# Kernel tuning notes

Measured on AMD Instinct MI355X. Metric: run time of the kernel, lower is better.

Reference implementation:

```python
import jax, jax.numpy as jnp
import numpy as np

B, S, D, H = 2, 2048, 1024, 16
ND = D // H  # head dim = 64


def setup_inputs() -> dict:
    key = jax.random.key(0)
    ks = jax.random.split(key, 11)
    scale = 1.0 / np.sqrt(D)
    inp = {
        "q": jax.random.normal(ks[0], (B, S, D), dtype=jnp.float32),
        "k": jax.random.normal(ks[1], (B, S, D), dtype=jnp.float32),
        "v": jax.random.normal(ks[2], (B, S, D), dtype=jnp.float32),
        # causal mask, broadcast over batch and heads
        "mask": jnp.tril(jnp.ones((S, S), dtype=jnp.int32))[None, None, :, :],
        "Wq": jax.random.normal(ks[3], (D, D), dtype=jnp.float32) * scale,
        "bq": jnp.zeros((D,), dtype=jnp.float32),
        "Wk": jax.random.normal(ks[4], (D, D), dtype=jnp.float32) * scale,
        "bk": jnp.zeros((D,), dtype=jnp.float32),
        "Wv": jax.random.normal(ks[5], (D, D), dtype=jnp.float32) * scale,
        "bv": jnp.zeros((D,), dtype=jnp.float32),
        "Wo": jax.random.normal(ks[6], (D, D), dtype=jnp.float32) * scale,
        "bo": jnp.zeros((D,), dtype=jnp.float32),
    }
    return inp


def reference(q, k, v, mask, Wq, bq, Wk, bk, Wv, bv, Wo, bo):
    batch, seq_len, _ = q.shape
    # torch nn.Linear: x @ W.T + b
    qh = (q @ Wq.T + bq).reshape(batch, seq_len, H, ND).transpose(0, 2, 1, 3)
    kh = (k @ Wk.T + bk).reshape(batch, seq_len, H, ND).transpose(0, 2, 1, 3)
    vh = (v @ Wv.T + bv).reshape(batch, seq_len, H, ND).transpose(0, 2, 1, 3)
    # [B,H,S,S] scores
    score = jnp.einsum("bhqd,bhkd->bhqk", qh, kh) / jnp.sqrt(jnp.float32(ND))
    score = jnp.where(mask == 0, jnp.float32(-1e9), score)
    score = jax.nn.softmax(score, axis=-1)
    out = jnp.einsum("bhqk,bhkd->bhqd", score, vh)
    out = out.transpose(0, 2, 1, 3).reshape(batch, seq_len, D)
    return out @ Wo.T + bo
```

## Files before the change

kernel.cpp:

```cpp
#include <hip/hip_runtime.h>
#include <hip/hip_bf16.h>
#include <stdint.h>

#define S_LEN 2048
#define DMODEL 1024
#define NHEAD 16
#define HDIM 64
#define BATCH 2

typedef __bf16 bf16_t;
typedef __attribute__((ext_vector_type(8))) __bf16 bf16x8;
typedef __attribute__((ext_vector_type(4))) __bf16 bf16x4;
typedef __attribute__((ext_vector_type(4))) float f32x4;

#define LOG2E 1.44269504088896340736f

__device__ __forceinline__ void gload_lds16(const void* g, void* l) {
  __builtin_amdgcn_global_load_lds(
      (const __attribute__((address_space(1))) uint32_t*)g,
      (__attribute__((address_space(3))) uint32_t*)l, 16, 0, 0);
}

__global__ __launch_bounds__(256) void convert_all(
    const float* __restrict__ q, const float* __restrict__ k, const float* __restrict__ v,
    const float* __restrict__ wq, const float* __restrict__ wk, const float* __restrict__ wv,
    const float* __restrict__ wo,
    bf16_t* __restrict__ qb, bf16_t* __restrict__ kb, bf16_t* __restrict__ vb,
    bf16_t* __restrict__ wqb, bf16_t* __restrict__ wkb, bf16_t* __restrict__ wvb,
    bf16_t* __restrict__ wob)
{
  const size_t M1 = 1048576;
  size_t e = ((size_t)blockIdx.x * 256 + threadIdx.x) * 4;
  const float* src; bf16_t* dst; size_t off;
  if      (e <  4*M1) { src = q;  dst = qb;  off = e;         }
  else if (e <  8*M1) { src = k;  dst = kb;  off = e - 4*M1;  }
  else if (e < 12*M1) { src = v;  dst = vb;  off = e - 8*M1;  }
  else if (e < 13*M1) { src = wq; dst = wqb; off = e - 12*M1; }
  else if (e < 14*M1) { src = wk; dst = wkb; off = e - 13*M1; }
  else if (e < 15*M1) { src = wv; dst = wvb; off = e - 14*M1; }
  else                { src = wo; dst = wob; off = e - 15*M1; }
  float4 f = *reinterpret_cast<const float4*>(src + off);
  bf16x4 o;
  o[0] = (bf16_t)f.x; o[1] = (bf16_t)f.y; o[2] = (bf16_t)f.z; o[3] = (bf16_t)f.w;
  *reinterpret_cast<bf16x4*>(dst + off) = o;
}

__device__ __forceinline__ void gemm_body(
    const bf16_t* __restrict__ A, const bf16_t* __restrict__ W,
    const float* __restrict__ bias, bf16_t* __restrict__ outb,
    float* __restrict__ outf, int M, int N, int K, float scale, int kpack)
{
  __shared__ bf16_t As[128 * 32];
  __shared__ bf16_t Bs[128 * 32];
  int tid = threadIdx.x;
  int w = tid >> 6, lane = tid & 63;
  int lr = lane & 15, lg = lane >> 4;
  int wr = w >> 1, wc = w & 1;
  int m0 = blockIdx.x * 128, n0 = blockIdx.y * 128;

  f32x4 acc[4][4];
#pragma unroll
  for (int a = 0; a < 4; ++a)
#pragma unroll
    for (int bq = 0; bq < 4; ++bq) acc[a][bq] = (f32x4){0.f, 0.f, 0.f, 0.f};

  int col_st = (lane & 3) * 8;

  for (int kt = 0; kt < K; kt += 32) {
#pragma unroll
    for (int it = 0; it < 2; ++it) {
      int chunkbase = (w * 2 + it) * 512;
      int row = (w * 2 + it) * 16 + (lane >> 2);
      gload_lds16(A + (size_t)(m0 + row) * K + kt + col_st, &As[chunkbase]);
      gload_lds16(W + (size_t)(n0 + row) * K + kt + col_st, &Bs[chunkbase]);
    }
    __syncthreads();
    bf16x8 af[4], bfv[4];
#pragma unroll
    for (int mf = 0; mf < 4; ++mf)
      af[mf] = *reinterpret_cast<const bf16x8*>(&As[(wr * 64 + mf * 16 + lr) * 32 + lg * 8]);
#pragma unroll
    for (int nf = 0; nf < 4; ++nf)
      bfv[nf] = *reinterpret_cast<const bf16x8*>(&Bs[(wc * 64 + nf * 16 + lr) * 32 + lg * 8]);
#pragma unroll
    for (int mf = 0; mf < 4; ++mf)
#pragma unroll
      for (int nf = 0; nf < 4; ++nf)
        acc[mf][nf] = __builtin_amdgcn_mfma_f32_16x16x32_bf16(af[mf], bfv[nf], acc[mf][nf], 0, 0, 0);
    __syncthreads();
  }

#pragma unroll
  for (int mf = 0; mf < 4; ++mf) {
#pragma unroll
    for (int nf = 0; nf < 4; ++nf) {
      int col = n0 + wc * 64 + nf * 16 + lr;
      float bcol = bias[col];
#pragma unroll
      for (int i = 0; i < 4; ++i) {
        int row = m0 + wr * 64 + mf * 16 + lg * 4 + i;
        float vv = (acc[mf][nf][i] + bcol) * scale;
        if (outf) {
          outf[(size_t)row * N + col] = vv;
        } else if (!kpack) {
          outb[(size_t)row * N + col] = (bf16_t)vv;
        } else {
          int hh = col >> 6, dh = col & 63;
          int half = dh >> 5, klg = (dh >> 3) & 3, j = dh & 7;
          int bb = row >> 11, s = row & 2047;
          size_t off = ((((size_t)(bb * 16 + hh) * 32 + (s >> 6)) * 4 + ((s >> 4) & 3)) * 2 + half) * 512
                     + (klg * 16 + (s & 15)) * 8 + j;
          outb[off] = (bf16_t)vv;
        }
      }
    }
  }
}

__global__ __launch_bounds__(256) void gemm_proj(
    const bf16_t* __restrict__ qb, const bf16_t* __restrict__ kb, const bf16_t* __restrict__ vb,
    const bf16_t* __restrict__ wqb, const bf16_t* __restrict__ wkb, const bf16_t* __restrict__ wvb,
    const float* __restrict__ bq, const float* __restrict__ bk, const float* __restrict__ bv,
    bf16_t* __restrict__ Qp, bf16_t* __restrict__ Kpk, bf16_t* __restrict__ Vp)
{
  int z = blockIdx.z;
  const bf16_t* A = (z == 0) ? qb : (z == 1) ? kb : vb;
  const bf16_t* W = (z == 0) ? wqb : (z == 1) ? wkb : wvb;
  const float* bias = (z == 0) ? bq : (z == 1) ? bk : bv;
  bf16_t* o = (z == 0) ? Qp : (z == 1) ? Kpk : Vp;
  float scale = (z == 0) ? 0.125f * LOG2E : 1.0f;
  gemm_body(A, W, bias, o, nullptr, BATCH * S_LEN, DMODEL, DMODEL, scale, z == 1);
}

__global__ __launch_bounds__(256) void gemm_out(
    const bf16_t* __restrict__ O, const bf16_t* __restrict__ wob,
    const float* __restrict__ bo, float* __restrict__ out)
{
  gemm_body(O, wob, bo, nullptr, out, BATCH * S_LEN, DMODEL, DMODEL, 1.0f, 0);
}

__global__ __launch_bounds__(256) void transpose_v(
    const bf16_t* __restrict__ Vp, bf16_t* __restrict__ Vpk)
{
  int bh = blockIdx.y, b = bh >> 4, h = bh & 15;
  int s0 = blockIdx.x * 64;
  __shared__ bf16_t lt[64 * 72];
  int tid = threadIdx.x;
  int c0 = (tid & 7) * 8;
#pragma unroll
  for (int it = 0; it < 2; ++it) {
    int rr = (tid >> 3) + it * 32;
    *reinterpret_cast<bf16x8*>(&lt[rr * 72 + c0]) =
        *reinterpret_cast<const bf16x8*>(Vp + ((size_t)b * S_LEN + s0 + rr) * DMODEL + h * HDIM + c0);
  }
  __syncthreads();
#pragma unroll
  for (int it = 0; it < 2; ++it) {
    int d = (tid >> 3) + it * 32;
    int sc = (tid & 7) * 8;
    bf16x8 o;
#pragma unroll
    for (int j = 0; j < 8; ++j) o[j] = lt[(sc + j) * 72 + d];
    int dfo = d >> 4, vlr = d & 15;
    int half = sc >> 5, vlg = (sc >> 3) & 3;
    size_t off = (((size_t)bh * 32 + blockIdx.x) * 8 + dfo * 2 + half) * 512
               + (vlg * 16 + vlr) * 8;
    *reinterpret_cast<bf16x8*>(Vpk + off) = o;
  }
}

#define PSTRIDE 66

__global__ __launch_bounds__(512, 4) void attn_fwd(
    const bf16_t* __restrict__ Qp, const bf16_t* __restrict__ Kpk,
    const bf16_t* __restrict__ Vpk, bf16_t* __restrict__ O)
{
  int flat = blockIdx.x;
  int low = flat & 7, kk = flat >> 3;
  int pj = kk & 15;
  int bh = ((kk >> 4) << 3) + low;
  int b = bh >> 4, h = bh & 15;
  int tid = threadIdx.x, wv = tid >> 6, lane = tid & 63;
  int lr = lane & 15, lg = lane >> 4;
  int grp = wv >> 2, wl = wv & 3;
  int qt = grp ? (31 - pj) : pj;

  __shared__ bf16_t Ps[8][16 * PSTRIDE];

  int q_row = qt * 64 + wl * 16 + lr;
  const bf16_t* Qbase = Qp + ((size_t)b * S_LEN + q_row) * DMODEL + h * HDIM + lg * 8;
  bf16x8 qf0 = *reinterpret_cast<const bf16x8*>(Qbase);
  bf16x8 qf1 = *reinterpret_cast<const bf16x8*>(Qbase + 32);

  f32x4 oacc[4];
#pragma unroll
  for (int df = 0; df < 4; ++df) oacc[df] = (f32x4){0.f, 0.f, 0.f, 0.f};
  float m = -1e30f, l = 0.f;

  const bf16_t* Kb = Kpk + (size_t)bh * (32 * 4096) + lane * 8;
  const bf16_t* Vb = Vpk + (size_t)bh * (32 * 4096) + lane * 8;
  bf16_t* ps = &Ps[wv][lr * PSTRIDE];

  for (int t = 0; t <= qt; ++t) {
    const bf16_t* Kt = Kb + t * 4096;
    const bf16_t* Vt_ = Vb + t * 4096;

    f32x4 sacc[4];
#pragma unroll
    for (int kvf = 0; kvf < 4; ++kvf) {
      bf16x8 kf0 = *reinterpret_cast<const bf16x8*>(Kt + (kvf * 2 + 0) * 512);
      bf16x8 kf1 = *reinterpret_cast<const bf16x8*>(Kt + (kvf * 2 + 1) * 512);
      f32x4 s = (f32x4){0.f, 0.f, 0.f, 0.f};
      s = __builtin_amdgcn_mfma_f32_16x16x32_bf16(kf0, qf0, s, 0, 0, 0);
      s = __builtin_amdgcn_mfma_f32_16x16x32_bf16(kf1, qf1, s, 0, 0, 0);
      sacc[kvf] = s;
    }

    bf16x8 vf[4][2];
#pragma unroll
    for (int dfo = 0; dfo < 4; ++dfo) {
      vf[dfo][0] = *reinterpret_cast<const bf16x8*>(Vt_ + (dfo * 2 + 0) * 512);
      vf[dfo][1] = *reinterpret_cast<const bf16x8*>(Vt_ + (dfo * 2 + 1) * 512);
    }

    if (t == qt) {
      int kv0 = t * 64;
#pragma unroll
      for (int kvf = 0; kvf < 4; ++kvf) {
        int kv_g = kv0 + kvf * 16 + lg * 4;
#pragma unroll
        for (int i = 0; i < 4; ++i)
          if (kv_g + i > q_row) sacc[kvf][i] = -1e30f;
      }
    }

    float lmax = fmaxf(fmaxf(sacc[0][0], sacc[0][1]), fmaxf(sacc[0][2], sacc[0][3]));
#pragma unroll
    for (int kvf = 1; kvf < 4; ++kvf)
      lmax = fmaxf(lmax, fmaxf(fmaxf(sacc[kvf][0], sacc[kvf][1]),
                               fmaxf(sacc[kvf][2], sacc[kvf][3])));
    if (__any(lmax > m + 8.f)) {
      float mx = lmax;
      mx = fmaxf(mx, __shfl_xor(mx, 16));
      mx = fmaxf(mx, __shfl_xor(mx, 32));
      float mn = fmaxf(m, mx);
      float rr = __builtin_amdgcn_exp2f(m - mn);
      m = mn; l *= rr;
#pragma unroll
      for (int dfo = 0; dfo < 4; ++dfo) oacc[dfo] *= rr;
    }

    float psum = 0.f;
#pragma unroll
    for (int kvf = 0; kvf < 4; ++kvf) {
      bf16x4 pw;
#pragma unroll
      for (int i = 0; i < 4; ++i) {
        float p = __builtin_amdgcn_exp2f(sacc[kvf][i] - m);
        psum += p;
        pw[i] = (bf16_t)p;
      }
      *reinterpret_cast<bf16x4*>(ps + kvf * 16 + lg * 4) = pw;
    }
    l += psum;

    asm volatile("s_waitcnt lgkmcnt(0)" ::: "memory");
    __builtin_amdgcn_sched_barrier(0);

    bf16x8 pa0 = *reinterpret_cast<const bf16x8*>(ps + lg * 8);
    bf16x8 pa1 = *reinterpret_cast<const bf16x8*>(ps + 32 + lg * 8);
#pragma unroll
    for (int dfo = 0; dfo < 4; ++dfo) {
      oacc[dfo] = __builtin_amdgcn_mfma_f32_16x16x32_bf16(vf[dfo][0], pa0, oacc[dfo], 0, 0, 0);
      oacc[dfo] = __builtin_amdgcn_mfma_f32_16x16x32_bf16(vf[dfo][1], pa1, oacc[dfo], 0, 0, 0);
    }
  }

  l += __shfl_xor(l, 16);
  l += __shfl_xor(l, 32);
  float inv = 1.0f / l;
  bf16_t* ob = O + ((size_t)b * S_LEN + q_row) * DMODEL + h * HDIM + lg * 4;
#pragma unroll
  for (int dfo = 0; dfo < 4; ++dfo) {
    bf16x4 ov;
#pragma unroll
    for (int i = 0; i < 4; ++i) ov[i] = (bf16_t)(oacc[dfo][i] * inv);
    *reinterpret_cast<bf16x4*>(ob + dfo * 16) = ov;
  }
}

extern "C" void kernel_launch(void* const* d_in, const int* in_sizes, int n_in,
                              void* d_out, int out_size, void* d_ws, size_t ws_size,
                              hipStream_t stream) {
  const float* q  = (const float*)d_in[0];
  const float* k  = (const float*)d_in[1];
  const float* v  = (const float*)d_in[2];
  const float* Wq = (const float*)d_in[4];
  const float* bq = (const float*)d_in[5];
  const float* Wk = (const float*)d_in[6];
  const float* bk = (const float*)d_in[7];
  const float* Wv = (const float*)d_in[8];
  const float* bv = (const float*)d_in[9];
  const float* Wo = (const float*)d_in[10];
  const float* bo = (const float*)d_in[11];
  float* out = (float*)d_out;

  const size_t MB = 1u << 20;
  char* base = (char*)d_ws;
  bf16_t* qb  = (bf16_t*)(base + 0 * MB);
  bf16_t* kb  = (bf16_t*)(base + 8 * MB);
  bf16_t* vb  = (bf16_t*)(base + 16 * MB);
  bf16_t* wqb = (bf16_t*)(base + 24 * MB);
  bf16_t* wkb = (bf16_t*)(base + 26 * MB);
  bf16_t* wvb = (bf16_t*)(base + 28 * MB);
  bf16_t* wob = (bf16_t*)(base + 30 * MB);
  bf16_t* Qp  = (bf16_t*)(base + 32 * MB);
  bf16_t* Kpk = (bf16_t*)(base + 40 * MB);
  bf16_t* Vp  = (bf16_t*)(base + 48 * MB);
  bf16_t* Vpk = (bf16_t*)(base + 56 * MB);
  bf16_t* Ob  = (bf16_t*)(base + 64 * MB);

  convert_all<<<16384, 256, 0, stream>>>(q, k, v, Wq, Wk, Wv, Wo,
                                         qb, kb, vb, wqb, wkb, wvb, wob);
  gemm_proj<<<dim3(32, 8, 3), 256, 0, stream>>>(qb, kb, vb, wqb, wkb, wvb,
                                                bq, bk, bv, Qp, Kpk, Vp);
  transpose_v<<<dim3(32, 32), 256, 0, stream>>>(Vp, Vpk);
  attn_fwd<<<512, 512, 0, stream>>>(Qp, Kpk, Vpk, Ob);
  gemm_out<<<dim3(32, 8), 256, 0, stream>>>(Ob, wob, bo, out);
}
```

Baseline: 134.8 us.

## Fuse V transpose into projection epilogue and prefetch K tiles in attention

The V projection GEMM now writes directly in the packed, transposed layout the attention kernel consumes, which removes the separate transpose_v kernel launch and its extra read/write of V. The attention loop also prefetches the next K tile into registers during softmax, so the load latency is hidden, and it raises wave priority around the MFMA blocks. The fused epilogue does scattered 2-byte stores with poor coalescing, and the K prefetch adds register pressure under a 4-waves launch bound.

```diff
diff --git a/kernel.cpp b/kernel.cpp
--- a/kernel.cpp
+++ b/kernel.cpp
@@ -48,7 +48,7 @@
 __device__ __forceinline__ void gemm_body(
     const bf16_t* __restrict__ A, const bf16_t* __restrict__ W,
     const float* __restrict__ bias, bf16_t* __restrict__ outb,
-    float* __restrict__ outf, int M, int N, int K, float scale, int kpack)
+    float* __restrict__ outf, int M, int N, int K, float scale, int packmode)
 {
   __shared__ bf16_t As[128 * 32];
   __shared__ bf16_t Bs[128 * 32];
@@ -102,15 +102,24 @@
         float vv = (acc[mf][nf][i] + bcol) * scale;
         if (outf) {
           outf[(size_t)row * N + col] = vv;
-        } else if (!kpack) {
+        } else if (packmode == 0) {
           outb[(size_t)row * N + col] = (bf16_t)vv;
-        } else {
+        } else if (packmode == 1) {
           int hh = col >> 6, dh = col & 63;
           int half = dh >> 5, klg = (dh >> 3) & 3, j = dh & 7;
           int bb = row >> 11, s = row & 2047;
           size_t off = ((((size_t)(bb * 16 + hh) * 32 + (s >> 6)) * 4 + ((s >> 4) & 3)) * 2 + half) * 512
                      + (klg * 16 + (s & 15)) * 8 + j;
           outb[off] = (bf16_t)vv;
+        } else {
+          int hh = col >> 6, d = col & 63;
+          int dfo = d >> 4, vlr = d & 15;
+          int bb = row >> 11, s = row & 2047;
+          int t64 = s >> 6, sin_ = s & 63;
+          int half = sin_ >> 5, vlg = (sin_ >> 3) & 3, j = s & 7;
+          size_t off = (((size_t)(bb * 16 + hh) * 32 + t64) * 8 + dfo * 2 + half) * 512
+                     + (vlg * 16 + vlr) * 8 + j;
+          outb[off] = (bf16_t)vv;
         }
       }
     }
@@ -121,15 +130,15 @@
     const bf16_t* __restrict__ qb, const bf16_t* __restrict__ kb, const bf16_t* __restrict__ vb,
     const bf16_t* __restrict__ wqb, const bf16_t* __restrict__ wkb, const bf16_t* __restrict__ wvb,
     const float* __restrict__ bq, const float* __restrict__ bk, const float* __restrict__ bv,
-    bf16_t* __restrict__ Qp, bf16_t* __restrict__ Kpk, bf16_t* __restrict__ Vp)
+    bf16_t* __restrict__ Qp, bf16_t* __restrict__ Kpk, bf16_t* __restrict__ Vpk)
 {
   int z = blockIdx.z;
   const bf16_t* A = (z == 0) ? qb : (z == 1) ? kb : vb;
   const bf16_t* W = (z == 0) ? wqb : (z == 1) ? wkb : wvb;
   const float* bias = (z == 0) ? bq : (z == 1) ? bk : bv;
-  bf16_t* o = (z == 0) ? Qp : (z == 1) ? Kpk : Vp;
+  bf16_t* o = (z == 0) ? Qp : (z == 1) ? Kpk : Vpk;
   float scale = (z == 0) ? 0.125f * LOG2E : 1.0f;
-  gemm_body(A, W, bias, o, nullptr, BATCH * S_LEN, DMODEL, DMODEL, scale, z == 1);
+  gemm_body(A, W, bias, o, nullptr, BATCH * S_LEN, DMODEL, DMODEL, scale, z);
 }
 
 __global__ __launch_bounds__(256) void gemm_out(
@@ -137,36 +146,6 @@
     const float* __restrict__ bo, float* __restrict__ out)
 {
   gemm_body(O, wob, bo, nullptr, out, BATCH * S_LEN, DMODEL, DMODEL, 1.0f, 0);
-}
-
-__global__ __launch_bounds__(256) void transpose_v(
-    const bf16_t* __restrict__ Vp, bf16_t* __restrict__ Vpk)
-{
-  int bh = blockIdx.y, b = bh >> 4, h = bh & 15;
-  int s0 = blockIdx.x * 64;
-  __shared__ bf16_t lt[64 * 72];
-  int tid = threadIdx.x;
-  int c0 = (tid & 7) * 8;
-#pragma unroll
-  for (int it = 0; it < 2; ++it) {
-    int rr = (tid >> 3) + it * 32;
-    *reinterpret_cast<bf16x8*>(&lt[rr * 72 + c0]) =
-        *reinterpret_cast<const bf16x8*>(Vp + ((size_t)b * S_LEN + s0 + rr) * DMODEL + h * HDIM + c0);
-  }
-  __syncthreads();
-#pragma unroll
-  for (int it = 0; it < 2; ++it) {
-    int d = (tid >> 3) + it * 32;
-    int sc = (tid & 7) * 8;
-    bf16x8 o;
-#pragma unroll
-    for (int j = 0; j < 8; ++j) o[j] = lt[(sc + j) * 72 + d];
-    int dfo = d >> 4, vlr = d & 15;
-    int half = sc >> 5, vlg = (sc >> 3) & 3;
-    size_t off = (((size_t)bh * 32 + blockIdx.x) * 8 + dfo * 2 + half) * 512
-               + (vlg * 16 + vlr) * 8;
-    *reinterpret_cast<bf16x8*>(Vpk + off) = o;
-  }
 }
 
 #define PSTRIDE 66
@@ -201,27 +180,31 @@
   const bf16_t* Vb = Vpk + (size_t)bh * (32 * 4096) + lane * 8;
   bf16_t* ps = &Ps[wv][lr * PSTRIDE];
 
+  bf16x8 kc[8];
+  {
+    const bf16_t* Kt = Kb;
+#pragma unroll
+    for (int f = 0; f < 8; ++f) kc[f] = *reinterpret_cast<const bf16x8*>(Kt + f * 512);
+  }
+
   for (int t = 0; t <= qt; ++t) {
-    const bf16_t* Kt = Kb + t * 4096;
     const bf16_t* Vt_ = Vb + t * 4096;
 
     f32x4 sacc[4];
+    __builtin_amdgcn_s_setprio(1);
 #pragma unroll
     for (int kvf = 0; kvf < 4; ++kvf) {
-      bf16x8 kf0 = *reinterpret_cast<const bf16x8*>(Kt + (kvf * 2 + 0) * 512);
-      bf16x8 kf1 = *reinterpret_cast<const bf16x8*>(Kt + (kvf * 2 + 1) * 512);
       f32x4 s = (f32x4){0.f, 0.f, 0.f, 0.f};
-      s = __builtin_amdgcn_mfma_f32_16x16x32_bf16(kf0, qf0, s, 0, 0, 0);
-      s = __builtin_amdgcn_mfma_f32_16x16x32_bf16(kf1, qf1, s, 0, 0, 0);
+      s = __builtin_amdgcn_mfma_f32_16x16x32_bf16(kc[kvf * 2 + 0], qf0, s, 0, 0, 0);
+      s = __builtin_amdgcn_mfma_f32_16x16x32_bf16(kc[kvf * 2 + 1], qf1, s, 0, 0, 0);
       sacc[kvf] = s;
     }
-
-    bf16x8 vf[4][2];
-#pragma unroll
-    for (int dfo = 0; dfo < 4; ++dfo) {
-      vf[dfo][0] = *reinterpret_cast<const bf16x8*>(Vt_ + (dfo * 2 + 0) * 512);
-      vf[dfo][1] = *reinterpret_cast<const bf16x8*>(Vt_ + (dfo * 2 + 1) * 512);
-    }
+    __builtin_amdgcn_s_setprio(0);
+
+    bf16x8 vf[8];
+#pragma unroll
+    for (int f = 0; f < 8; ++f)
+      vf[f] = *reinterpret_cast<const bf16x8*>(Vt_ + f * 512);
 
     if (t == qt) {
       int kv0 = t * 64;
@@ -264,16 +247,24 @@
     }
     l += psum;
 
+    if (t + 1 <= qt) {
+      const bf16_t* Kt = Kb + (t + 1) * 4096;
+#pragma unroll
+      for (int f = 0; f < 8; ++f) kc[f] = *reinterpret_cast<const bf16x8*>(Kt + f * 512);
+    }
+
     asm volatile("s_waitcnt lgkmcnt(0)" ::: "memory");
     __builtin_amdgcn_sched_barrier(0);
 
     bf16x8 pa0 = *reinterpret_cast<const bf16x8*>(ps + lg * 8);
     bf16x8 pa1 = *reinterpret_cast<const bf16x8*>(ps + 32 + lg * 8);
+    __builtin_amdgcn_s_setprio(1);
 #pragma unroll
     for (int dfo = 0; dfo < 4; ++dfo) {
-      oacc[dfo] = __builtin_amdgcn_mfma_f32_16x16x32_bf16(vf[dfo][0], pa0, oacc[dfo], 0, 0, 0);
-      oacc[dfo] = __builtin_amdgcn_mfma_f32_16x16x32_bf16(vf[dfo][1], pa1, oacc[dfo], 0, 0, 0);
-    }
+      oacc[dfo] = __builtin_amdgcn_mfma_f32_16x16x32_bf16(vf[dfo * 2 + 0], pa0, oacc[dfo], 0, 0, 0);
+      oacc[dfo] = __builtin_amdgcn_mfma_f32_16x16x32_bf16(vf[dfo * 2 + 1], pa1, oacc[dfo], 0, 0, 0);
+    }
+    __builtin_amdgcn_s_setprio(0);
   }
 
   l += __shfl_xor(l, 16);
@@ -316,15 +307,13 @@
   bf16_t* wob = (bf16_t*)(base + 30 * MB);
   bf16_t* Qp  = (bf16_t*)(base + 32 * MB);
   bf16_t* Kpk = (bf16_t*)(base + 40 * MB);
-  bf16_t* Vp  = (bf16_t*)(base + 48 * MB);
   bf16_t* Vpk = (bf16_t*)(base + 56 * MB);
   bf16_t* Ob  = (bf16_t*)(base + 64 * MB);
 
   convert_all<<<16384, 256, 0, stream>>>(q, k, v, Wq, Wk, Wv, Wo,
                                          qb, kb, vb, wqb, wkb, wvb, wob);
   gemm_proj<<<dim3(32, 8, 3), 256, 0, stream>>>(qb, kb, vb, wqb, wkb, wvb,
-                                                bq, bk, bv, Qp, Kpk, Vp);
-  transpose_v<<<dim3(32, 32), 256, 0, stream>>>(Vp, Vpk);
+                                                bq, bk, bv, Qp, Kpk, Vpk);
   attn_fwd<<<512, 512, 0, stream>>>(Qp, Kpk, Vpk, Ob);
   gemm_out<<<dim3(32, 8), 256, 0, stream>>>(Ob, wob, bo, out);
 }
```

After: 131.1 us. -2.7%, faster.
